# Performance work log

Measured on AMD Instinct MI355X. Metric: run time of the kernel, lower is better.

The kernel has to match this reference:

```python
import jax, jax.numpy as jnp
import numpy as np

B, C, H, W = 1, 512, 24, 24
N_HEADS, WS = 8, 7
PAD = WS // 2
HEAD_DIM = C // N_HEADS


def setup_inputs() -> dict:
    key = jax.random.key(0)
    ks = jax.random.split(key, 7)
    s = 0.02
    return {
        "x": jax.random.normal(ks[0], (B, C, H, W), dtype=jnp.float32),
        "Wq": s * jax.random.normal(ks[1], (C, C), dtype=jnp.float32),
        "bq": s * jax.random.normal(ks[2], (C,), dtype=jnp.float32),
        "Wk": s * jax.random.normal(ks[3], (C, C), dtype=jnp.float32),
        "bk": s * jax.random.normal(ks[4], (C,), dtype=jnp.float32),
        "Wv": s * jax.random.normal(ks[5], (C, C), dtype=jnp.float32),
        "bv": s * jax.random.normal(ks[6], (C,), dtype=jnp.float32),
        # module initializes gamma to zero; use small nonzero so output depends on attention
        "gamma": jnp.full((1,), 0.1, dtype=jnp.float32),
    }


def _conv1x1(z, Wt, bt):
    # 1x1 Conv2d == per-pixel GEMM over channels
    return jnp.einsum("bchw,oc->bohw", z, Wt) + bt[None, :, None, None]


def _windows(z):
    # z: (B, C, H+ws-1, W+ws-1) -> (B, n_heads, head_dim, ws*ws*H*W)
    # matches torch unfold(2,ws,1).unfold(3,ws,1).permute(0,1,4,5,2,3).view(...)
    taps = [z[:, :, di:di + H, dj:dj + W] for di in range(WS) for dj in range(WS)]
    w = jnp.stack(taps, axis=2)  # (B, C, ws*ws, H, W)
    return w.reshape(B, N_HEADS, HEAD_DIM, WS * WS * H * W)


def reference(x, Wq, bq, Wk, bk, Wv, bv, gamma):
    q = _conv1x1(x, Wq, bq).reshape(B, N_HEADS, HEAD_DIM, H * W)  # (B,h,d,HW)
    xp = jnp.pad(x, ((0, 0), (0, 0), (PAD, PAD), (PAD, PAD)), mode="reflect")
    k = _windows(_conv1x1(xp, Wk, bk))  # (B,h,d,ws^2*HW)
    v = _windows(_conv1x1(xp, Wv, bv))  # (B,h,d,ws^2*HW)
    # NOTE: as written in the source, each query attends to ALL ws^2*H*W keys
    energy = jnp.einsum("bhdq,bhdk->bhqk", q, k)  # (B,h,HW,ws^2*HW)
    attn = jax.nn.softmax(energy, axis=-1)
    out_w = jnp.einsum("bhqk,bhdk->bhdq", attn, v).reshape(B, C, H, W)
    return gamma * out_w + x
```

## Files before the change

kernel.cpp:

```cpp
#include <hip/hip_runtime.h>

#define HW   576
#define CC   512
#define PW   30
#define PPK  1024
#define NS   4
#define SP   256

typedef float f32x4 __attribute__((ext_vector_type(4)));
typedef short s16x8 __attribute__((ext_vector_type(8)));

__device__ __forceinline__ unsigned short f2bf(float f) {
    unsigned u = __float_as_uint(f);
    return (unsigned short)((u + 0x7FFFu + ((u >> 16) & 1u)) >> 16);
}
__device__ __forceinline__ float bf2f(unsigned short h) {
    return __uint_as_float((unsigned)h << 16);
}
__device__ __forceinline__ int smapf(int p) {
    if (p >= 900) return 576;
    const int y = p / PW, xw = p - y * PW;
    int iy = y - 3;  iy = (iy < 0) ? -iy : (iy > 23 ? 46 - iy : iy);
    int ix = xw - 3; ix = (ix < 0) ? -ix : (ix > 23 ? 46 - ix : ix);
    return iy * 24 + ix;
}

#define OFF_QT 0u
#define OFF_KT 589824u
#define OFF_VP 1638400u
#define OFF_MP 2686976u
#define OFF_LP 2760704u
#define OFF_OP 2834432u
#define OFF_XT 5193728u
#define OFF_WB 5784576u

__global__ __launch_bounds__(256) void cvtT(
    const float* __restrict__ x,
    const float* __restrict__ Wq, const float* __restrict__ Wk,
    const float* __restrict__ Wv,
    unsigned short* __restrict__ xT, unsigned short* __restrict__ wb)
{
    const int b = blockIdx.x, t = threadIdx.x;
    if (b < 72) {
        __shared__ float tile[64][65];
        const int pt = b % 9, ct = b / 9;
        const int p0 = pt * 64, c0 = ct * 64;
        const int tr = t >> 4, tc4 = (t & 15) * 4;
        #pragma unroll
        for (int cr = 0; cr < 4; ++cr) {
            const int row = cr * 16 + tr;
            const float4 v = *(const float4*)&x[(size_t)(c0 + row) * HW + p0 + tc4];
            tile[row][tc4 + 0] = v.x;
            tile[row][tc4 + 1] = v.y;
            tile[row][tc4 + 2] = v.z;
            tile[row][tc4 + 3] = v.w;
        }
        __syncthreads();
        #pragma unroll
        for (int cr = 0; cr < 4; ++cr) {
            const int prow = cr * 16 + tr;
            ushort4 o;
            o.x = f2bf(tile[tc4 + 0][prow]);
            o.y = f2bf(tile[tc4 + 1][prow]);
            o.z = f2bf(tile[tc4 + 2][prow]);
            o.w = f2bf(tile[tc4 + 3][prow]);
            *(ushort4*)&xT[(size_t)(p0 + prow) * CC + c0 + tc4] = o;
        }
    } else if (b == 72) {
        if (t < 128) *(ushort4*)&xT[(size_t)576 * CC + t * 4] = (ushort4){0, 0, 0, 0};
    } else {
        const int wi = (b - 73) * 2048 + t * 8;
        const int sel = wi >> 18, off = wi & 262143;
        const float* src = (sel == 0) ? Wq : (sel == 1) ? Wk : Wv;
        const float4 v0 = *(const float4*)&src[off];
        const float4 v1 = *(const float4*)&src[off + 4];
        ushort4 o0, o1;
        o0.x = f2bf(v0.x); o0.y = f2bf(v0.y); o0.z = f2bf(v0.z); o0.w = f2bf(v0.w);
        o1.x = f2bf(v1.x); o1.y = f2bf(v1.y); o1.z = f2bf(v1.z); o1.w = f2bf(v1.w);
        *(ushort4*)&wb[wi]     = o0;
        *(ushort4*)&wb[wi + 4] = o1;
    }
}

__global__ __launch_bounds__(256) void qkv_direct(
    const unsigned short* __restrict__ xT, const unsigned short* __restrict__ wb,
    const float* __restrict__ bq, const float* __restrict__ bk,
    const float* __restrict__ bv,
    unsigned short* __restrict__ qT, unsigned short* __restrict__ kT,
    unsigned short* __restrict__ vP)
{
    const int t = threadIdx.x;
    const int w = blockIdx.x * 4 + (t >> 6);
    const int lane = t & 63, fr = lane & 15, u = lane >> 4;

    int sel, m0, n0;
    if (w < 576)       { sel = 0; m0 = (w >> 4) << 4;               n0 = (w & 15) << 5; }
    else if (w < 1600) { const int k = w - 576;  sel = 1; m0 = (k >> 4) << 4; n0 = (k & 15) << 5; }
    else               { const int k = w - 1600; sel = 2; m0 = (k >> 5) << 4; n0 = (k & 31) << 5; }

    const unsigned short *A, *B;
    int ar, bn0, bn1;
    if (sel == 0)      { A = xT;          B = wb;          ar = m0 + fr;
                         bn0 = n0 + fr;          bn1 = n0 + 16 + fr; }
    else if (sel == 1) { A = xT;          B = wb + 262144; ar = smapf(m0 + fr);
                         bn0 = n0 + fr;          bn1 = n0 + 16 + fr; }
    else               { A = wb + 524288; B = xT;          ar = m0 + fr;
                         bn0 = smapf(n0 + fr);   bn1 = smapf(n0 + 16 + fr); }

    const unsigned short* Ap  = A + (size_t)ar  * CC + u * 8;
    const unsigned short* Bp0 = B + (size_t)bn0 * CC + u * 8;
    const unsigned short* Bp1 = B + (size_t)bn1 * CC + u * 8;

    f32x4 acc0 = (f32x4){0.f, 0.f, 0.f, 0.f};
    f32x4 acc1 = (f32x4){0.f, 0.f, 0.f, 0.f};
    #pragma unroll 8
    for (int k0 = 0; k0 < CC; k0 += 32) {
        const s16x8 a  = *(const s16x8*)(Ap  + k0);
        const s16x8 b0 = *(const s16x8*)(Bp0 + k0);
        const s16x8 b1 = *(const s16x8*)(Bp1 + k0);
        acc0 = __builtin_amdgcn_mfma_f32_16x16x32_bf16(a, b0, acc0, 0, 0, 0);
        acc1 = __builtin_amdgcn_mfma_f32_16x16x32_bf16(a, b1, acc1, 0, 0, 0);
    }

    #pragma unroll
    for (int ni = 0; ni < 2; ++ni) {
        const f32x4 acc = ni ? acc1 : acc0;
        #pragma unroll
        for (int r = 0; r < 4; ++r) {
            const int m = m0 + u * 4 + r;
            const int n = n0 + ni * 16 + fr;
            if (sel == 0) {
                qT[((size_t)(n >> 6) * HW + m) * 64 + (n & 63)] = f2bf(acc[r] + bq[n]);
            } else if (sel == 1) {
                kT[((size_t)(n >> 6) * PPK + m) * 64 + (n & 63)] = f2bf(acc[r] + bk[n]);
            } else {
                vP[((size_t)(m >> 6) * 64 + (m & 63)) * PPK + n] = f2bf(acc[r] + bv[m]);
            }
        }
    }
}

__global__ __launch_bounds__(256) void attn3(
    const unsigned short* __restrict__ qT, const unsigned short* __restrict__ kT,
    const unsigned short* __restrict__ vP, float* __restrict__ mP,
    float* __restrict__ lP, unsigned short* __restrict__ Op)
{
    const int q0 = blockIdx.x * 16;
    const int s  = blockIdx.y;
    const int hd = blockIdx.z;
    const int t  = threadIdx.x;
    const int lane = t & 63, w = t >> 6;
    const int fr = lane & 15, u = lane >> 4;

    __shared__ float cnt_s[SP];
    __shared__ __align__(16) unsigned short Wl[16 * 272];
    __shared__ float mw[64], lw[64];

    if (t < SP) {
        const int p = s * SP + t;
        float c = 0.f;
        if (p < 900) {
            const int y = p / PW, xw = p - y * PW;
            int cy = y + 1;  if (PW - y  < cy) cy = PW - y;  if (cy > 7) cy = 7;
            int cx = xw + 1; if (PW - xw < cx) cx = PW - xw; if (cx > 7) cx = 7;
            c = (float)(cy * cx);
        }
        cnt_s[t] = c;
    }

    const unsigned short* qrow = qT + ((size_t)hd * HW + q0 + fr) * 64 + u * 8;
    const s16x8 b0 = *(const s16x8*)qrow;
    const s16x8 b1 = *(const s16x8*)(qrow + 32);

    f32x4 e[4];
    #pragma unroll
    for (int t4 = 0; t4 < 4; ++t4) {
        const unsigned short* krow =
            kT + ((size_t)hd * PPK + s * SP + w * 64 + t4 * 16 + fr) * 64 + u * 8;
        const s16x8 a0 = *(const s16x8*)krow;
        const s16x8 a1 = *(const s16x8*)(krow + 32);
        f32x4 a = (f32x4){0.f, 0.f, 0.f, 0.f};
        a = __builtin_amdgcn_mfma_f32_16x16x32_bf16(a0, b0, a, 0, 0, 0);
        a = __builtin_amdgcn_mfma_f32_16x16x32_bf16(a1, b1, a, 0, 0, 0);
        e[t4] = a;
    }

    float m = -1e30f;
    #pragma unroll
    for (int t4 = 0; t4 < 4; ++t4)
        #pragma unroll
        for (int r = 0; r < 4; ++r) m = fmaxf(m, e[t4][r]);
    m = fmaxf(m, __shfl_xor(m, 16));
    m = fmaxf(m, __shfl_xor(m, 32));
    if (lane < 16) mw[w * 16 + lane] = m;
    __syncthreads();
    const float mq = fmaxf(fmaxf(mw[fr], mw[16 + fr]), fmaxf(mw[32 + fr], mw[48 + fr]));

    float sum = 0.f;
    #pragma unroll
    for (int t4 = 0; t4 < 4; ++t4) {
        unsigned short wb4[4];
        #pragma unroll
        for (int r = 0; r < 4; ++r) {
            const float wv2 = cnt_s[w * 64 + t4 * 16 + u * 4 + r] *
                              __expf(e[t4][r] - mq);
            sum += wv2;
            wb4[r] = f2bf(wv2);
        }
        const int ho = fr * 272 + w * 64 + t4 * 16 + u * 4;
        *(unsigned*)&Wl[ho]     = (unsigned)wb4[0] | ((unsigned)wb4[1] << 16);
        *(unsigned*)&Wl[ho + 2] = (unsigned)wb4[2] | ((unsigned)wb4[3] << 16);
    }
    sum += __shfl_xor(sum, 16);
    sum += __shfl_xor(sum, 32);
    if (lane < 16) lw[w * 16 + lane] = sum;
    __syncthreads();

    if (t < 16) {
        const float lq = lw[t] + lw[16 + t] + lw[32 + t] + lw[48 + t];
        const float mq2 = fmaxf(fmaxf(mw[t], mw[16 + t]),
                                fmaxf(mw[32 + t], mw[48 + t]));
        const int si = (hd * NS + s) * HW + q0 + t;
        lP[si] = lq;
        mP[si] = mq2;
    }

    f32x4 o = (f32x4){0.f, 0.f, 0.f, 0.f};
    const unsigned short* vrow =
        vP + ((size_t)hd * 64 + w * 16 + fr) * PPK + s * SP + u * 8;
    #pragma unroll
    for (int c = 0; c < 8; ++c) {
        const s16x8 aw = *(const s16x8*)&Wl[fr * 272 + c * 32 + u * 8];
        const s16x8 bv2 = *(const s16x8*)(vrow + c * 32);
        o = __builtin_amdgcn_mfma_f32_16x16x32_bf16(aw, bv2, o, 0, 0, 0);
    }
    #pragma unroll
    for (int r = 0; r < 4; ++r) {
        const size_t oi =
            ((size_t)(hd * NS + s) * HW + q0 + u * 4 + r) * 64 + w * 16 + fr;
        Op[oi] = f2bf(o[r]);
    }
}

__global__ __launch_bounds__(256) void combine2(
    const unsigned short* __restrict__ Op, const float* __restrict__ mP,
    const float* __restrict__ lP, const float* __restrict__ x,
    const float* __restrict__ gamma, float* __restrict__ out)
{
    const int hd = blockIdx.y;
    const int q  = blockIdx.x * 64 + (threadIdx.x >> 2);
    const int dq = (threadIdx.x & 3) * 16;

    const int sb = (hd * NS) * HW + q;
    const float m0 = mP[sb], m1 = mP[sb + HW];
    const float m2 = mP[sb + 2 * HW], m3 = mP[sb + 3 * HW];
    const float ms = fmaxf(fmaxf(m0, m1), fmaxf(m2, m3));
    const float a[NS] = {__expf(m0 - ms), __expf(m1 - ms),
                         __expf(m2 - ms), __expf(m3 - ms)};
    const float l = lP[sb] * a[0] + lP[sb + HW] * a[1] +
                    lP[sb + 2 * HW] * a[2] + lP[sb + 3 * HW] * a[3];
    const float scale = gamma[0] / l;

    float o[16] = {};
    #pragma unroll
    for (int s = 0; s < NS; ++s) {
        const unsigned short* op = &Op[((size_t)(sb + s * HW)) * 64 + dq];
        const uint4 u0 = *(const uint4*)op;
        const uint4 u1 = *(const uint4*)(op + 8);
        const unsigned uu[8] = {u0.x, u0.y, u0.z, u0.w, u1.x, u1.y, u1.z, u1.w};
        #pragma unroll
        for (int j = 0; j < 8; ++j) {
            o[2 * j]     = fmaf(a[s], bf2f((unsigned short)(uu[j] & 0xFFFF)), o[2 * j]);
            o[2 * j + 1] = fmaf(a[s], bf2f((unsigned short)(uu[j] >> 16)),    o[2 * j + 1]);
        }
    }
    #pragma unroll
    for (int i = 0; i < 16; ++i) {
        const size_t gi = (size_t)(hd * 64 + dq + i) * HW + q;
        out[gi] = fmaf(scale, o[i], x[gi]);
    }
}

extern "C" void kernel_launch(void* const* d_in, const int* in_sizes, int n_in,
                              void* d_out, int out_size, void* d_ws, size_t ws_size,
                              hipStream_t stream) {
    const float* x     = (const float*)d_in[0];
    const float* Wq    = (const float*)d_in[1];
    const float* bq    = (const float*)d_in[2];
    const float* Wk    = (const float*)d_in[3];
    const float* bk    = (const float*)d_in[4];
    const float* Wv    = (const float*)d_in[5];
    const float* bv    = (const float*)d_in[6];
    const float* gamma = (const float*)d_in[7];
    float* out = (float*)d_out;

    char* wsb = (char*)d_ws;
    unsigned short* qT = (unsigned short*)(wsb + OFF_QT);
    unsigned short* kT = (unsigned short*)(wsb + OFF_KT);
    unsigned short* vP = (unsigned short*)(wsb + OFF_VP);
    float*          mP = (float*)(wsb + OFF_MP);
    float*          lP = (float*)(wsb + OFF_LP);
    unsigned short* Op = (unsigned short*)(wsb + OFF_OP);
    unsigned short* xT = (unsigned short*)(wsb + OFF_XT);
    unsigned short* wb = (unsigned short*)(wsb + OFF_WB);

    cvtT<<<dim3(457), 256, 0, stream>>>(x, Wq, Wk, Wv, xT, wb);
    qkv_direct<<<dim3(656), 256, 0, stream>>>(xT, wb, bq, bk, bv, qT, kT, vP);
    attn3<<<dim3(36, NS, 8), 256, 0, stream>>>(qT, kT, vP, mP, lP, Op);
    combine2<<<dim3(9, 8), 256, 0, stream>>>(Op, mP, lP, x, gamma, out);
}
```

Baseline: 107.8 us.

## Fuse split-key attention and combine into one 512-thread kernel

Replaces the four-way split over keys plus a separate combine kernel with a single attention kernel. Each block of 8 waves covers all 1024 keys for 16 queries and reduces the two half-range PV partials through shared memory. It then applies gamma, the softmax normalization and the residual directly. This removes a kernel launch and the round trip of partial outputs, max and sum values through global memory. The grid shrinks from 1152 to 288 blocks and shared memory per block grows, which lowers parallelism on a large GPU.

```diff
diff --git a/kernel.cpp b/kernel.cpp
--- a/kernel.cpp
+++ b/kernel.cpp
@@ -4,8 +4,7 @@
 #define CC   512
 #define PW   30
 #define PPK  1024
-#define NS   4
-#define SP   256
+#define WLS  1048
 
 typedef float f32x4 __attribute__((ext_vector_type(4)));
 typedef short s16x8 __attribute__((ext_vector_type(8)));
@@ -28,11 +27,8 @@
 #define OFF_QT 0u
 #define OFF_KT 589824u
 #define OFF_VP 1638400u
-#define OFF_MP 2686976u
-#define OFF_LP 2760704u
-#define OFF_OP 2834432u
-#define OFF_XT 5193728u
-#define OFF_WB 5784576u
+#define OFF_XT 2686976u
+#define OFF_WB 3277824u
 
 __global__ __launch_bounds__(256) void cvtT(
     const float* __restrict__ x,
@@ -140,144 +136,121 @@
     }
 }
 
-__global__ __launch_bounds__(256) void attn3(
+__global__ __launch_bounds__(512) void attn4(
     const unsigned short* __restrict__ qT, const unsigned short* __restrict__ kT,
-    const unsigned short* __restrict__ vP, float* __restrict__ mP,
-    float* __restrict__ lP, unsigned short* __restrict__ Op)
+    const unsigned short* __restrict__ vP, const float* __restrict__ x,
+    const float* __restrict__ gamma, float* __restrict__ out)
 {
+    const int hd = blockIdx.y;
     const int q0 = blockIdx.x * 16;
-    const int s  = blockIdx.y;
-    const int hd = blockIdx.z;
     const int t  = threadIdx.x;
-    const int lane = t & 63, w = t >> 6;
+    const int w = t >> 6, lane = t & 63;
     const int fr = lane & 15, u = lane >> 4;
 
-    __shared__ float cnt_s[SP];
-    __shared__ __align__(16) unsigned short Wl[16 * 272];
-    __shared__ float mw[64], lw[64];
-
-    if (t < SP) {
-        const int p = s * SP + t;
+    __shared__ float cnt_s[PPK];
+    __shared__ __align__(16) unsigned short Wl[16 * WLS];
+    __shared__ float mw[128], lw[128], red[16];
+    __shared__ __align__(16) float Osc[8][64][4];
+
+    for (int i = t; i < PPK; i += 512) {
         float c = 0.f;
-        if (p < 900) {
-            const int y = p / PW, xw = p - y * PW;
+        if (i < 900) {
+            const int y = i / PW, xw = i - y * PW;
             int cy = y + 1;  if (PW - y  < cy) cy = PW - y;  if (cy > 7) cy = 7;
             int cx = xw + 1; if (PW - xw < cx) cx = PW - xw; if (cx > 7) cx = 7;
             c = (float)(cy * cx);
         }
-        cnt_s[t] = c;
+        cnt_s[i] = c;
     }
 
     const unsigned short* qrow = qT + ((size_t)hd * HW + q0 + fr) * 64 + u * 8;
     const s16x8 b0 = *(const s16x8*)qrow;
     const s16x8 b1 = *(const s16x8*)(qrow + 32);
 
-    f32x4 e[4];
-    #pragma unroll
-    for (int t4 = 0; t4 < 4; ++t4) {
+    f32x4 e[8];
+    #pragma unroll
+    for (int t8 = 0; t8 < 8; ++t8) {
         const unsigned short* krow =
-            kT + ((size_t)hd * PPK + s * SP + w * 64 + t4 * 16 + fr) * 64 + u * 8;
+            kT + ((size_t)hd * PPK + w * 128 + t8 * 16 + fr) * 64 + u * 8;
         const s16x8 a0 = *(const s16x8*)krow;
         const s16x8 a1 = *(const s16x8*)(krow + 32);
         f32x4 a = (f32x4){0.f, 0.f, 0.f, 0.f};
         a = __builtin_amdgcn_mfma_f32_16x16x32_bf16(a0, b0, a, 0, 0, 0);
         a = __builtin_amdgcn_mfma_f32_16x16x32_bf16(a1, b1, a, 0, 0, 0);
-        e[t4] = a;
+        e[t8] = a;
     }
 
     float m = -1e30f;
     #pragma unroll
-    for (int t4 = 0; t4 < 4; ++t4)
-        #pragma unroll
-        for (int r = 0; r < 4; ++r) m = fmaxf(m, e[t4][r]);
+    for (int t8 = 0; t8 < 8; ++t8)
+        #pragma unroll
+        for (int r = 0; r < 4; ++r) m = fmaxf(m, e[t8][r]);
     m = fmaxf(m, __shfl_xor(m, 16));
     m = fmaxf(m, __shfl_xor(m, 32));
     if (lane < 16) mw[w * 16 + lane] = m;
     __syncthreads();
-    const float mq = fmaxf(fmaxf(mw[fr], mw[16 + fr]), fmaxf(mw[32 + fr], mw[48 + fr]));
+    float mq = mw[fr];
+    #pragma unroll
+    for (int w2 = 1; w2 < 8; ++w2) mq = fmaxf(mq, mw[w2 * 16 + fr]);
 
     float sum = 0.f;
     #pragma unroll
-    for (int t4 = 0; t4 < 4; ++t4) {
+    for (int t8 = 0; t8 < 8; ++t8) {
+        const int pb = w * 128 + t8 * 16 + u * 4;
         unsigned short wb4[4];
         #pragma unroll
         for (int r = 0; r < 4; ++r) {
-            const float wv2 = cnt_s[w * 64 + t4 * 16 + u * 4 + r] *
-                              __expf(e[t4][r] - mq);
-            sum += wv2;
-            wb4[r] = f2bf(wv2);
-        }
-        const int ho = fr * 272 + w * 64 + t4 * 16 + u * 4;
-        *(unsigned*)&Wl[ho]     = (unsigned)wb4[0] | ((unsigned)wb4[1] << 16);
-        *(unsigned*)&Wl[ho + 2] = (unsigned)wb4[2] | ((unsigned)wb4[3] << 16);
+            const float wv = cnt_s[pb + r] * __expf(e[t8][r] - mq);
+            sum += wv;
+            wb4[r] = f2bf(wv);
+        }
+        const unsigned lo = (unsigned)wb4[0] | ((unsigned)wb4[1] << 16);
+        const unsigned hi = (unsigned)wb4[2] | ((unsigned)wb4[3] << 16);
+        *(unsigned long long*)&Wl[fr * WLS + pb] =
+            (unsigned long long)lo | ((unsigned long long)hi << 32);
     }
     sum += __shfl_xor(sum, 16);
     sum += __shfl_xor(sum, 32);
     if (lane < 16) lw[w * 16 + lane] = sum;
     __syncthreads();
-
     if (t < 16) {
-        const float lq = lw[t] + lw[16 + t] + lw[32 + t] + lw[48 + t];
-        const float mq2 = fmaxf(fmaxf(mw[t], mw[16 + t]),
-                                fmaxf(mw[32 + t], mw[48 + t]));
-        const int si = (hd * NS + s) * HW + q0 + t;
-        lP[si] = lq;
-        mP[si] = mq2;
-    }
-
+        float l = lw[t];
+        #pragma unroll
+        for (int w2 = 1; w2 < 8; ++w2) l += lw[w2 * 16 + t];
+        red[t] = l;
+    }
+
+    const int dt = w & 3, hp = w >> 2;
     f32x4 o = (f32x4){0.f, 0.f, 0.f, 0.f};
     const unsigned short* vrow =
-        vP + ((size_t)hd * 64 + w * 16 + fr) * PPK + s * SP + u * 8;
-    #pragma unroll
-    for (int c = 0; c < 8; ++c) {
-        const s16x8 aw = *(const s16x8*)&Wl[fr * 272 + c * 32 + u * 8];
+        vP + ((size_t)hd * 64 + dt * 16 + fr) * PPK + hp * 512 + u * 8;
+    const unsigned short* wrow = &Wl[fr * WLS + hp * 512 + u * 8];
+    #pragma unroll
+    for (int c = 0; c < 16; ++c) {
+        const s16x8 aw  = *(const s16x8*)(wrow + c * 32);
         const s16x8 bv2 = *(const s16x8*)(vrow + c * 32);
         o = __builtin_amdgcn_mfma_f32_16x16x32_bf16(aw, bv2, o, 0, 0, 0);
     }
-    #pragma unroll
-    for (int r = 0; r < 4; ++r) {
-        const size_t oi =
-            ((size_t)(hd * NS + s) * HW + q0 + u * 4 + r) * 64 + w * 16 + fr;
-        Op[oi] = f2bf(o[r]);
-    }
-}
-
-__global__ __launch_bounds__(256) void combine2(
-    const unsigned short* __restrict__ Op, const float* __restrict__ mP,
-    const float* __restrict__ lP, const float* __restrict__ x,
-    const float* __restrict__ gamma, float* __restrict__ out)
-{
-    const int hd = blockIdx.y;
-    const int q  = blockIdx.x * 64 + (threadIdx.x >> 2);
-    const int dq = (threadIdx.x & 3) * 16;
-
-    const int sb = (hd * NS) * HW + q;
-    const float m0 = mP[sb], m1 = mP[sb + HW];
-    const float m2 = mP[sb + 2 * HW], m3 = mP[sb + 3 * HW];
-    const float ms = fmaxf(fmaxf(m0, m1), fmaxf(m2, m3));
-    const float a[NS] = {__expf(m0 - ms), __expf(m1 - ms),
-                         __expf(m2 - ms), __expf(m3 - ms)};
-    const float l = lP[sb] * a[0] + lP[sb + HW] * a[1] +
-                    lP[sb + 2 * HW] * a[2] + lP[sb + 3 * HW] * a[3];
-    const float scale = gamma[0] / l;
-
-    float o[16] = {};
-    #pragma unroll
-    for (int s = 0; s < NS; ++s) {
-        const unsigned short* op = &Op[((size_t)(sb + s * HW)) * 64 + dq];
-        const uint4 u0 = *(const uint4*)op;
-        const uint4 u1 = *(const uint4*)(op + 8);
-        const unsigned uu[8] = {u0.x, u0.y, u0.z, u0.w, u1.x, u1.y, u1.z, u1.w};
-        #pragma unroll
-        for (int j = 0; j < 8; ++j) {
-            o[2 * j]     = fmaf(a[s], bf2f((unsigned short)(uu[j] & 0xFFFF)), o[2 * j]);
-            o[2 * j + 1] = fmaf(a[s], bf2f((unsigned short)(uu[j] >> 16)),    o[2 * j + 1]);
-        }
-    }
-    #pragma unroll
-    for (int i = 0; i < 16; ++i) {
-        const size_t gi = (size_t)(hd * 64 + dq + i) * HW + q;
-        out[gi] = fmaf(scale, o[i], x[gi]);
+    *(float4*)&Osc[w][lane][0] = make_float4(o[0], o[1], o[2], o[3]);
+    __syncthreads();
+
+    {
+        const int d = t >> 3, qp = (t & 7) * 2;
+        const int dt2 = d >> 4, frd = d & 15;
+        const float g = gamma[0];
+        float2 r2;
+        #pragma unroll
+        for (int j = 0; j < 2; ++j) {
+            const int q = qp + j;
+            const int ln = (q >> 2) * 16 + frd, rq = q & 3;
+            const float val = Osc[dt2][ln][rq] + Osc[dt2 + 4][ln][rq];
+            (&r2.x)[j] = (g / red[q]) * val;
+        }
+        const size_t gi = (size_t)(hd * 64 + d) * HW + q0 + qp;
+        const float2 xi = *(const float2*)&x[gi];
+        r2.x += xi.x;
+        r2.y += xi.y;
+        *(float2*)&out[gi] = r2;
     }
 }
 
@@ -298,14 +271,10 @@
     unsigned short* qT = (unsigned short*)(wsb + OFF_QT);
     unsigned short* kT = (unsigned short*)(wsb + OFF_KT);
     unsigned short* vP = (unsigned short*)(wsb + OFF_VP);
-    float*          mP = (float*)(wsb + OFF_MP);
-    float*          lP = (float*)(wsb + OFF_LP);
-    unsigned short* Op = (unsigned short*)(wsb + OFF_OP);
     unsigned short* xT = (unsigned short*)(wsb + OFF_XT);
     unsigned short* wb = (unsigned short*)(wsb + OFF_WB);
 
     cvtT<<<dim3(457), 256, 0, stream>>>(x, Wq, Wk, Wv, xT, wb);
     qkv_direct<<<dim3(656), 256, 0, stream>>>(xT, wb, bq, bk, bv, qT, kT, vP);
-    attn3<<<dim3(36, NS, 8), 256, 0, stream>>>(qT, kT, vP, mP, lP, Op);
-    combine2<<<dim3(9, 8), 256, 0, stream>>>(Op, mP, lP, x, gamma, out);
-}
+    attn4<<<dim3(36, 8), 512, 0, stream>>>(qT, kT, vP, x, gamma, out);
+}
```

Result: no change. 109.0 us (+1.1%).
